# Kernel tuning notes

Hardware: AMD Instinct MI355X
Metric: run time of the kernel (lower is better)

## Reference

```python
import jax, jax.numpy as jnp
import numpy as np

SEARCH_RANGE = 4  # max_displacement == pad in tfa CorrelationCost


def setup_inputs() -> dict:
    key = jax.random.key(0)
    k1, k2 = jax.random.split(key)
    B, C, H, W = 4, 128, 128, 256
    prv = jax.random.normal(k1, (B, C, H, W), dtype=jnp.float32)
    nxt = jax.random.normal(k2, (B, C, H, W), dtype=jnp.float32)
    return {"prv": prv, "nxt": nxt}


def reference(prv, nxt):
    """tfa CorrelationCost with kernel_size=1, stride_1=stride_2=1,
    max_displacement=pad=SEARCH_RANGE, channels_first.

    out[b, k, y, x] = (1/C) * sum_c prv[b,c,y,x] * nxt_pad[b,c,y+dy,x+dx]
    with k = (dy+d)*(2d+1) + (dx+d) (dy outer loop, dx inner, as in the
    tfa CUDA kernel), nxt zero-padded by d on each spatial side.
    """
    d = SEARCH_RANGE
    B, C, H, W = prv.shape
    nd = 2 * d + 1  # neighborhood width -> nd*nd output channels
    nxt_pad = jnp.pad(nxt, ((0, 0), (0, 0), (d, d), (d, d)))
    inv_c = jnp.float32(1.0 / C)
    outs = []
    # fixed small loop over (2d+1)^2 = 81 displacement offsets
    for dy in range(nd):
        for dx in range(nd):
            shifted = jax.lax.dynamic_slice(nxt_pad, (0, 0, dy, dx), (B, C, H, W))
            # reduce over channels: [B, H, W]
            outs.append(jnp.einsum('bchw,bchw->bhw', prv, shifted) * inv_c)
    return jnp.stack(outs, axis=1)  # [B, 81, H, W]
```

## Files before the change

kernel.cpp:

```cpp
#include <hip/hip_runtime.h>


#define SR 4
#define ND 9
#define BB 4
#define CC 128
#define HH 128
#define WW 256
#define HW (HH * WW)
#define PADW 264
#define RSTR 40

typedef __fp16 h2 __attribute__((ext_vector_type(2)));

static __device__ __forceinline__ h2 pk(float lo, float hi) {
    return __builtin_amdgcn_cvt_pkrtz(lo, hi);
}
static __device__ __forceinline__ h2 as_h2(unsigned u) {
    union { unsigned u; h2 h; } v; v.u = u; return v.h;
}
static __device__ __forceinline__ unsigned as_u32(h2 h) {
    union { unsigned u; h2 h; } v; v.h = h; return v.u;
}

#define CFENCE asm volatile("" ::: "memory")

__global__ __launch_bounds__(256, 3) void costvol_kernel(
    const float* __restrict__ prv,
    const float* __restrict__ nxt,
    float* __restrict__ out)
{
    __shared__ unsigned shraw[4 * 2 * 3 * PADW];

    const int nwg  = gridDim.x;
    const int cpx  = nwg >> 3;
    const int orig = blockIdx.x;
    const int wid  = (orig & 7) * cpx + (orig >> 3);

    const int g  = wid % 3;
    const int r_ = wid / 3;
    const int yp = r_ & 63;
    const int b  = r_ >> 6;

    const int tid  = threadIdx.x;
    const int w    = tid >> 6;
    const int lane = tid & 63;
    const int ry   = w & 1;
    const int ch   = w >> 1;
    const int x0   = lane << 2;
    const int y    = (yp << 1) + ry;
    const int r0   = y + 3 * g - SR;

    bool vok[3];
    #pragma unroll
    for (int j = 0; j < 3; ++j)
        vok[j] = ((unsigned)(r0 + j) < (unsigned)HH);

    unsigned* stg = shraw + w * (2 * 3 * PADW);

    if (lane < 12) {
        const int e  = lane >= 6 ? 1 : 0;
        const int q  = lane - 6 * e;
        const int bf = q & 1;
        const int j  = q >> 1;
        *reinterpret_cast<uint4*>(stg + (bf * 3 + j) * PADW + (e ? 260 : 0)) =
            make_uint4(0u, 0u, 0u, 0u);
    }

    const size_t cbase = (size_t)(b * CC + (ch << 6)) * HW;
    const float* pg = prv + cbase + (size_t)y * WW + x0;
    const float* ng = nxt + cbase + (ptrdiff_t)r0 * WW + x0;

    float acc[3][ND][4];
    #pragma unroll
    for (int j = 0; j < 3; ++j)
        #pragma unroll
        for (int dx = 0; dx < ND; ++dx)
            #pragma unroll
            for (int px = 0; px < 4; ++px)
                acc[j][dx][px] = 0.f;

    #define LOADP(k, P0, P1, N) do { \
        const float* pp_ = pg + (size_t)(2 * (k)) * HW; \
        P0 = *reinterpret_cast<const float4*>(pp_); \
        P1 = *reinterpret_cast<const float4*>(pp_ + HW); \
        const float* nn_ = ng + (size_t)(2 * (k)) * HW; \
        _Pragma("unroll") \
        for (int j_ = 0; j_ < 3; ++j_) { \
            if (vok[j_]) { \
                N[j_][0] = *reinterpret_cast<const float4*>(nn_ + j_ * WW); \
                N[j_][1] = *reinterpret_cast<const float4*>(nn_ + j_ * WW + HW); \
            } else { \
                N[j_][0] = make_float4(0.f, 0.f, 0.f, 0.f); \
                N[j_][1] = make_float4(0.f, 0.f, 0.f, 0.f); \
            } \
        } } while (0)

    #define PKN(NH, N) do { \
        _Pragma("unroll") \
        for (int j_ = 0; j_ < 3; ++j_) { \
            NH[j_][0] = as_u32(pk(N[j_][0].x, N[j_][1].x)); \
            NH[j_][1] = as_u32(pk(N[j_][0].y, N[j_][1].y)); \
            NH[j_][2] = as_u32(pk(N[j_][0].z, N[j_][1].z)); \
            NH[j_][3] = as_u32(pk(N[j_][0].w, N[j_][1].w)); \
        } } while (0)

    #define STAGE(bf, NH) do { \
        _Pragma("unroll") \
        for (int j_ = 0; j_ < 3; ++j_) \
            *reinterpret_cast<uint4*>(stg + ((bf) * 3 + j_) * PADW + 4 + x0) = \
                make_uint4(NH[j_][0], NH[j_][1], NH[j_][2], NH[j_][3]); \
        } while (0)

    float4 P0c, P1c, P0n, P1n, Nc[3][2], Nn[3][2];
    unsigned nhc[3][4], nhn[3][4];

    LOADP(0, P0c, P1c, Nc);
    PKN(nhc, Nc);
    STAGE(0, nhc);
    CFENCE;

    for (int k = 0; k < 32; ++k) {
        const int bf = k & 1;
        if (k < 31) LOADP(k + 1, P0n, P1n, Nn);

        h2 ph[4];
        ph[0] = pk(P0c.x, P1c.x); ph[1] = pk(P0c.y, P1c.y);
        ph[2] = pk(P0c.z, P1c.z); ph[3] = pk(P0c.w, P1c.w);

        #pragma unroll
        for (int j = 0; j < 3; ++j) {
            const unsigned* row = stg + (bf * 3 + j) * PADW;
            const uint4 wl = *reinterpret_cast<const uint4*>(row + x0);
            const uint4 wr = *reinterpret_cast<const uint4*>(row + x0 + 8);
            h2 n12[12];
            n12[0] = as_h2(wl.x); n12[1] = as_h2(wl.y);
            n12[2] = as_h2(wl.z); n12[3] = as_h2(wl.w);
            n12[4] = as_h2(nhc[j][0]); n12[5] = as_h2(nhc[j][1]);
            n12[6] = as_h2(nhc[j][2]); n12[7] = as_h2(nhc[j][3]);
            n12[8] = as_h2(wr.x); n12[9] = as_h2(wr.y);
            n12[10] = as_h2(wr.z); n12[11] = as_h2(wr.w);
            #pragma unroll
            for (int dx = 0; dx < ND; ++dx)
                #pragma unroll
                for (int px = 0; px < 4; ++px)
                    acc[j][dx][px] =
                        __builtin_amdgcn_fdot2(ph[px], n12[dx + px], acc[j][dx][px], false);
        }

        if (k < 31) {
            PKN(nhn, Nn);
            STAGE(bf ^ 1, nhn);
            CFENCE;
            P0c = P0n; P1c = P1n;
            #pragma unroll
            for (int j = 0; j < 3; ++j)
                #pragma unroll
                for (int i = 0; i < 4; ++i)
                    nhc[j][i] = nhn[j][i];
        }
    }
    #undef STAGE
    #undef PKN
    #undef LOADP

    const float invc = 1.0f / (float)CC;
    #pragma unroll
    for (int j = 0; j < 3; ++j) {
        __syncthreads();
        if (ch == 1) {
            float* red = reinterpret_cast<float*>(shraw) + ((ry << 6) + lane) * RSTR;
            #pragma unroll
            for (int dx = 0; dx < ND; ++dx)
                *reinterpret_cast<float4*>(red + (dx << 2)) =
                    make_float4(acc[j][dx][0], acc[j][dx][1],
                                acc[j][dx][2], acc[j][dx][3]);
        }
        __syncthreads();
        if (ch == 0) {
            const float* red = reinterpret_cast<const float*>(shraw) + ((ry << 6) + lane) * RSTR;
            const int dy = 3 * g + j;
            #pragma unroll
            for (int dx = 0; dx < ND; ++dx) {
                const float4 t = *reinterpret_cast<const float4*>(red + (dx << 2));
                float* op = out + ((size_t)(b * 81 + dy * ND + dx) * HH + y) * WW + x0;
                *reinterpret_cast<float4*>(op) = make_float4(
                    (acc[j][dx][0] + t.x) * invc, (acc[j][dx][1] + t.y) * invc,
                    (acc[j][dx][2] + t.z) * invc, (acc[j][dx][3] + t.w) * invc);
            }
        }
    }
}

extern "C" void kernel_launch(void* const* d_in, const int* in_sizes, int n_in,
                              void* d_out, int out_size, void* d_ws, size_t ws_size,
                              hipStream_t stream) {
    const float* prv = (const float*)d_in[0];
    const float* nxt = (const float*)d_in[1];
    float* out = (float*)d_out;

    const int nblocks = BB * (HH / 2) * 3;
    costvol_kernel<<<nblocks, 256, 0, stream>>>(prv, nxt, out);
}
```

Before: 50.75 us.

## Split channel reduction across four waves per row instead of two rows

Each workgroup now handles a single output row, with its four waves each covering 32 channels instead of two rows times 64 channels. This doubles the grid to shorten each wave's serial channel loop and raise parallelism. In exchange it adds a two-stage shared-memory tree reduction with extra barriers, and more redundant loading of neighbor rows across workgroups. The reduction stride is also reduced.

```diff
diff --git a/kernel.cpp b/kernel.cpp
--- a/kernel.cpp
+++ b/kernel.cpp
@@ -9,7 +9,7 @@
 #define WW 256
 #define HW (HH * WW)
 #define PADW 264
-#define RSTR 40
+#define RSTR 36
 
 typedef __fp16 h2 __attribute__((ext_vector_type(2)));
 
@@ -39,16 +39,13 @@
 
     const int g  = wid % 3;
     const int r_ = wid / 3;
-    const int yp = r_ & 63;
-    const int b  = r_ >> 6;
+    const int y  = r_ & 127;
+    const int b  = r_ >> 7;
 
     const int tid  = threadIdx.x;
     const int w    = tid >> 6;
     const int lane = tid & 63;
-    const int ry   = w & 1;
-    const int ch   = w >> 1;
     const int x0   = lane << 2;
-    const int y    = (yp << 1) + ry;
     const int r0   = y + 3 * g - SR;
 
     bool vok[3];
@@ -67,7 +64,7 @@
             make_uint4(0u, 0u, 0u, 0u);
     }
 
-    const size_t cbase = (size_t)(b * CC + (ch << 6)) * HW;
+    const size_t cbase = (size_t)(b * CC + (w << 5)) * HW;
     const float* pg = prv + cbase + (size_t)y * WW + x0;
     const float* ng = nxt + cbase + (ptrdiff_t)r0 * WW + x0;
 
@@ -120,9 +117,9 @@
     STAGE(0, nhc);
     CFENCE;
 
-    for (int k = 0; k < 32; ++k) {
+    for (int k = 0; k < 16; ++k) {
         const int bf = k & 1;
-        if (k < 31) LOADP(k + 1, P0n, P1n, Nn);
+        if (k < 15) LOADP(k + 1, P0n, P1n, Nn);
 
         h2 ph[4];
         ph[0] = pk(P0c.x, P1c.x); ph[1] = pk(P0c.y, P1c.y);
@@ -148,7 +145,7 @@
                         __builtin_amdgcn_fdot2(ph[px], n12[dx + px], acc[j][dx][px], false);
         }
 
-        if (k < 31) {
+        if (k < 15) {
             PKN(nhn, Nn);
             STAGE(bf ^ 1, nhn);
             CFENCE;
@@ -165,24 +162,44 @@
     #undef LOADP
 
     const float invc = 1.0f / (float)CC;
+    float* red = reinterpret_cast<float*>(shraw);
     #pragma unroll
     for (int j = 0; j < 3; ++j) {
-        __syncthreads();
-        if (ch == 1) {
-            float* red = reinterpret_cast<float*>(shraw) + ((ry << 6) + lane) * RSTR;
+        const int dy = 3 * g + j;
+        __syncthreads();
+        if (w & 1) {
+            float* rp = red + (((w >> 1) << 6) + lane) * RSTR;
             #pragma unroll
             for (int dx = 0; dx < ND; ++dx)
-                *reinterpret_cast<float4*>(red + (dx << 2)) =
+                *reinterpret_cast<float4*>(rp + (dx << 2)) =
                     make_float4(acc[j][dx][0], acc[j][dx][1],
                                 acc[j][dx][2], acc[j][dx][3]);
         }
         __syncthreads();
-        if (ch == 0) {
-            const float* red = reinterpret_cast<const float*>(shraw) + ((ry << 6) + lane) * RSTR;
-            const int dy = 3 * g + j;
+        if (!(w & 1)) {
+            const float* rp = red + (((w >> 1) << 6) + lane) * RSTR;
             #pragma unroll
             for (int dx = 0; dx < ND; ++dx) {
-                const float4 t = *reinterpret_cast<const float4*>(red + (dx << 2));
+                const float4 t = *reinterpret_cast<const float4*>(rp + (dx << 2));
+                acc[j][dx][0] += t.x; acc[j][dx][1] += t.y;
+                acc[j][dx][2] += t.z; acc[j][dx][3] += t.w;
+            }
+        }
+        __syncthreads();
+        if (w == 2) {
+            float* rp = red + lane * RSTR;
+            #pragma unroll
+            for (int dx = 0; dx < ND; ++dx)
+                *reinterpret_cast<float4*>(rp + (dx << 2)) =
+                    make_float4(acc[j][dx][0], acc[j][dx][1],
+                                acc[j][dx][2], acc[j][dx][3]);
+        }
+        __syncthreads();
+        if (w == 0) {
+            const float* rp = red + lane * RSTR;
+            #pragma unroll
+            for (int dx = 0; dx < ND; ++dx) {
+                const float4 t = *reinterpret_cast<const float4*>(rp + (dx << 2));
                 float* op = out + ((size_t)(b * 81 + dy * ND + dx) * HH + y) * WW + x0;
                 *reinterpret_cast<float4*>(op) = make_float4(
                     (acc[j][dx][0] + t.x) * invc, (acc[j][dx][1] + t.y) * invc,
@@ -199,6 +216,6 @@
     const float* nxt = (const float*)d_in[1];
     float* out = (float*)d_out;
 
-    const int nblocks = BB * (HH / 2) * 3;
+    const int nblocks = BB * HH * 3;
     costvol_kernel<<<nblocks, 256, 0, stream>>>(prv, nxt, out);
 }
```

Measured after the change: 53.23 us. 4.9% more time.
